# Kernel tuning notes

Hardware: AMD Instinct MI355X
Metric: run time of the kernel (lower is better)

Reference implementation:

```python
import jax, jax.numpy as jnp
import numpy as np

B = 8192

def setup_inputs() -> dict:
    key = jax.random.key(0)
    k1, k2, k3 = jax.random.split(key, 3)
    pred = jax.random.normal(k1, (B,), dtype=jnp.float32)
    frac_time = jax.random.uniform(k2, (B,), dtype=jnp.float32) * 100.0
    if_mof = (jax.random.uniform(k3, (B,)) < 0.7).astype(jnp.float32)  # 0/1 flags
    gt = jnp.stack([frac_time, if_mof], axis=1)  # [B, 2]
    return {"pred": pred, "gt": gt, "gt_fracTime": 0, "gt_ifMOF": 1}


def reference(pred, gt, gt_fracTime, gt_ifMOF):
    # pred: [B], gt: [B,2]
    target = gt[:, gt_fracTime]          # [B]
    if_mof = gt[:, gt_ifMOF]             # [B], 0/1 flags
    flag = (if_mof == 1).astype(pred.dtype)
    n = pred.shape[0]
    # valid pairs: i < j with both flags set (loss term is symmetric in (i,j))
    triu = jnp.triu(jnp.ones((n, n), dtype=bool), k=1)
    pair_mask = (flag[:, None] * flag[None, :]) * triu.astype(pred.dtype)  # [B,B]
    dp = pred[:, None] - pred[None, :]      # [B,B]
    dt = target[:, None] - target[None, :]  # [B,B]
    loss = jnp.maximum(dp * dt / 100.0, 0.0)
    n_pairs = pair_mask.sum()
    return (loss * pair_mask).sum() / n_pairs
```

## Files before the change

kernel.cpp:

```cpp
#include <hip/hip_runtime.h>

#define NELEM 8192
#define JTILE 32
#define NJT   (NELEM / JTILE)
#define IPT   16
#define IBLK  (256 * IPT)
#define NIB   (NELEM / IBLK)
#define NBLK  (NIB * NJT)
#define SCB   NBLK

__global__ __launch_bounds__(256) void cindex_fused(
    const float* __restrict__ pred,
    const float* __restrict__ gt,
    const int* __restrict__ colT,
    const int* __restrict__ colF,
    float* __restrict__ ws,
    unsigned int* __restrict__ counter,
    float* __restrict__ out)
{
    __shared__ float2 sj[JTILE];
    __shared__ float  wsum[4];
    __shared__ float  s5[4][5];
    __shared__ int    lastBlock;

    const int tid = threadIdx.x;
    const int ib  = blockIdx.x;
    const int tj  = blockIdx.y;
    const int ct  = colT[0];
    const int cf  = colF[0];

    if (tid < JTILE) {
        const int j = tj * JTILE + tid;
        const float2 g = ((const float2*)gt)[j];
        const float tv = (ct == 0) ? g.x : g.y;
        const float fv = (cf == 0) ? g.x : g.y;
        const float pj = pred[j];
        const bool  fl = (fv == 1.0f);
        sj[tid] = make_float2(fl ? pj : 0.0f, fl ? tv * 0.01f : 0.0f);
    }
    __syncthreads();

    float p[IPT], t[IPT], f[IPT], acc[IPT];
    #pragma unroll
    for (int k = 0; k < IPT; ++k) {
        const int i = ib * IBLK + k * 256 + tid;
        const float2 g = ((const float2*)gt)[i];
        p[k] = pred[i];
        t[k] = ((ct == 0) ? g.x : g.y) * 0.01f;
        f[k] = (((cf == 0) ? g.x : g.y) == 1.0f) ? 1.0f : 0.0f;
        acc[k] = 0.0f;
    }

    #pragma unroll 4
    for (int jj = 0; jj < JTILE; ++jj) {
        const float2 v = sj[jj];
        #pragma unroll
        for (int k = 0; k < IPT; ++k)
            acc[k] = fmaf(fabsf(p[k] - v.x), fabsf(t[k] - v.y), acc[k]);
    }

    float s = 0.0f;
    #pragma unroll
    for (int k = 0; k < IPT; ++k) s = fmaf(f[k], acc[k], s);
    for (int off = 32; off > 0; off >>= 1) s += __shfl_down(s, off, 64);
    if ((tid & 63) == 0) wsum[tid >> 6] = s;

    if (tj == 0) {
        float c = 0, sp = 0, st = 0, spt = 0, sab = 0;
        #pragma unroll
        for (int k = 0; k < IPT; ++k) {
            const float pt = p[k] * t[k];
            c   += f[k];
            sp   = fmaf(f[k], p[k], sp);
            st   = fmaf(f[k], t[k], st);
            spt  = fmaf(f[k], pt, spt);
            sab  = fmaf(f[k], fabsf(pt), sab);
        }
        for (int off = 32; off > 0; off >>= 1) {
            c   += __shfl_down(c,   off, 64);
            sp  += __shfl_down(sp,  off, 64);
            st  += __shfl_down(st,  off, 64);
            spt += __shfl_down(spt, off, 64);
            sab += __shfl_down(sab, off, 64);
        }
        if ((tid & 63) == 0) {
            const int w = tid >> 6;
            s5[w][0] = c;  s5[w][1] = sp;  s5[w][2] = st;
            s5[w][3] = spt; s5[w][4] = sab;
        }
    }
    __syncthreads();

    if (tid == 0) {
        const float bsum = wsum[0] + wsum[1] + wsum[2] + wsum[3];
        __hip_atomic_store(&ws[tj * NIB + ib], bsum,
                           __ATOMIC_RELAXED, __HIP_MEMORY_SCOPE_AGENT);
        if (tj == 0) {
            #pragma unroll
            for (int m = 0; m < 5; ++m)
                __hip_atomic_store(&ws[SCB + ib * 5 + m],
                                   s5[0][m] + s5[1][m] + s5[2][m] + s5[3][m],
                                   __ATOMIC_RELAXED, __HIP_MEMORY_SCOPE_AGENT);
        }
        const unsigned old = __hip_atomic_fetch_add(counter, 1u,
                                __ATOMIC_ACQ_REL, __HIP_MEMORY_SCOPE_AGENT);
        lastBlock = ((old & (NBLK - 1)) == NBLK - 1) ? 1 : 0;
    }
    __syncthreads();
    if (!lastBlock) return;

    double d = 0.0;
    for (int i = tid; i < NBLK; i += 256)
        d += (double)__hip_atomic_load(&ws[i],
                        __ATOMIC_RELAXED, __HIP_MEMORY_SCOPE_AGENT);
    for (int off = 32; off > 0; off >>= 1) d += __shfl_down(d, off, 64);
    __shared__ double sd[4];
    if ((tid & 63) == 0) sd[tid >> 6] = d;
    __syncthreads();
    if (tid == 0) {
        const double Braw = sd[0] + sd[1] + sd[2] + sd[3];
        double M = 0, P = 0, Q = 0, T = 0, D = 0;
        for (int ibb = 0; ibb < NIB; ++ibb) {
            const float* o = ws + SCB + ibb * 5;
            M += (double)__hip_atomic_load(&o[0], __ATOMIC_RELAXED, __HIP_MEMORY_SCOPE_AGENT);
            P += (double)__hip_atomic_load(&o[1], __ATOMIC_RELAXED, __HIP_MEMORY_SCOPE_AGENT);
            Q += (double)__hip_atomic_load(&o[2], __ATOMIC_RELAXED, __HIP_MEMORY_SCOPE_AGENT);
            T += (double)__hip_atomic_load(&o[3], __ATOMIC_RELAXED, __HIP_MEMORY_SCOPE_AGENT);
            D += (double)__hip_atomic_load(&o[4], __ATOMIC_RELAXED, __HIP_MEMORY_SCOPE_AGENT);
        }
        const double A = 2.0 * (M * T - P * Q);
        const double B = Braw - ((double)NELEM - M) * D;
        out[0] = (float)((A + B) / (2.0 * M * (M - 1.0)));
    }
}

extern "C" void kernel_launch(void* const* d_in, const int* in_sizes, int n_in,
                              void* d_out, int out_size, void* d_ws, size_t ws_size,
                              hipStream_t stream) {
    const float* pred = (const float*)d_in[0];
    const float* gt   = (const float*)d_in[1];
    const int*   colT = (const int*)d_in[2];
    const int*   colF = (const int*)d_in[3];

    float* ws = (float*)d_ws;
    unsigned int* counter = (unsigned int*)(ws + 1024);

    dim3 grid(NIB, NJT);
    cindex_fused<<<grid, 256, 0, stream>>>(pred, gt, colT, colF, ws,
                                           counter, (float*)d_out);
}
```

Measured before the change: 20.16 us.

## Use hierarchical group counters for last-block detection and vectorize i-loads

Swaps the single global arrival counter for per-group counters of 64 blocks, each padded to its own cache line. Only the last block of each group touches a final counter, which is meant to cut contention among 512 blocks hitting one atomic. Per-thread element loads also become contiguous float4 loads instead of strided scalar loads. The change in which elements each thread owns does not affect the sum but changes access coalescing across a warp.

```diff
diff --git a/kernel.cpp b/kernel.cpp
--- a/kernel.cpp
+++ b/kernel.cpp
@@ -8,6 +8,10 @@
 #define NIB   (NELEM / IBLK)
 #define NBLK  (NIB * NJT)
 #define SCB   NBLK
+#define GRPSZ 64
+#define NGRP  (NBLK / GRPSZ)
+#define CNTB  1024
+#define FINC  (CNTB + NGRP * 64)
 
 __global__ __launch_bounds__(256) void cindex_fused(
     const float* __restrict__ pred,
@@ -15,7 +19,6 @@
     const int* __restrict__ colT,
     const int* __restrict__ colF,
     float* __restrict__ ws,
-    unsigned int* __restrict__ counter,
     float* __restrict__ out)
 {
     __shared__ float2 sj[JTILE];
@@ -26,6 +29,7 @@
     const int tid = threadIdx.x;
     const int ib  = blockIdx.x;
     const int tj  = blockIdx.y;
+    const int bid = tj * NIB + ib;
     const int ct  = colT[0];
     const int cf  = colF[0];
 
@@ -41,14 +45,26 @@
     __syncthreads();
 
     float p[IPT], t[IPT], f[IPT], acc[IPT];
-    #pragma unroll
-    for (int k = 0; k < IPT; ++k) {
-        const int i = ib * IBLK + k * 256 + tid;
-        const float2 g = ((const float2*)gt)[i];
-        p[k] = pred[i];
-        t[k] = ((ct == 0) ? g.x : g.y) * 0.01f;
-        f[k] = (((cf == 0) ? g.x : g.y) == 1.0f) ? 1.0f : 0.0f;
-        acc[k] = 0.0f;
+    {
+        const int i0 = ib * IBLK + tid * IPT;
+        const float4* p4 = (const float4*)(pred + i0);
+        const float4* g4 = (const float4*)(gt + 2 * i0);
+        float4 pr[IPT / 4], gr[IPT / 2];
+        #pragma unroll
+        for (int q = 0; q < IPT / 4; ++q) pr[q] = p4[q];
+        #pragma unroll
+        for (int q = 0; q < IPT / 2; ++q) gr[q] = g4[q];
+        #pragma unroll
+        for (int k = 0; k < IPT; ++k) {
+            p[k] = ((const float*)pr)[k];
+            const float gx = ((const float*)gr)[2 * k];
+            const float gy = ((const float*)gr)[2 * k + 1];
+            const float tv = (ct == 0) ? gx : gy;
+            const float fv = (cf == 0) ? gx : gy;
+            t[k] = tv * 0.01f;
+            f[k] = (fv == 1.0f) ? 1.0f : 0.0f;
+            acc[k] = 0.0f;
+        }
     }
 
     #pragma unroll 4
@@ -93,7 +109,7 @@
 
     if (tid == 0) {
         const float bsum = wsum[0] + wsum[1] + wsum[2] + wsum[3];
-        __hip_atomic_store(&ws[tj * NIB + ib], bsum,
+        __hip_atomic_store(&ws[bid], bsum,
                            __ATOMIC_RELAXED, __HIP_MEMORY_SCOPE_AGENT);
         if (tj == 0) {
             #pragma unroll
@@ -102,9 +118,17 @@
                                    s5[0][m] + s5[1][m] + s5[2][m] + s5[3][m],
                                    __ATOMIC_RELAXED, __HIP_MEMORY_SCOPE_AGENT);
         }
-        const unsigned old = __hip_atomic_fetch_add(counter, 1u,
+        unsigned int* grpCnt = (unsigned int*)&ws[CNTB + (bid / GRPSZ) * 64];
+        const unsigned old = __hip_atomic_fetch_add(grpCnt, 1u,
                                 __ATOMIC_ACQ_REL, __HIP_MEMORY_SCOPE_AGENT);
-        lastBlock = ((old & (NBLK - 1)) == NBLK - 1) ? 1 : 0;
+        int isFinal = 0;
+        if ((old & (GRPSZ - 1)) == GRPSZ - 1) {
+            unsigned int* finCnt = (unsigned int*)&ws[FINC];
+            const unsigned o2 = __hip_atomic_fetch_add(finCnt, 1u,
+                                    __ATOMIC_ACQ_REL, __HIP_MEMORY_SCOPE_AGENT);
+            isFinal = ((o2 & (NGRP - 1)) == NGRP - 1) ? 1 : 0;
+        }
+        lastBlock = isFinal;
     }
     __syncthreads();
     if (!lastBlock) return;
@@ -143,9 +167,7 @@
     const int*   colF = (const int*)d_in[3];
 
     float* ws = (float*)d_ws;
-    unsigned int* counter = (unsigned int*)(ws + 1024);
 
     dim3 grid(NIB, NJT);
-    cindex_fused<<<grid, 256, 0, stream>>>(pred, gt, colT, colF, ws,
-                                           counter, (float*)d_out);
+    cindex_fused<<<grid, 256, 0, stream>>>(pred, gt, colT, colF, ws, (float*)d_out);
 }
```

New measurement: 21.02 us. 4.3% more time.
